# Kernel tuning notes

Measured on AMD Instinct MI355X. Metric: run time of the kernel, lower is better.

Reference implementation:

```python
import jax, jax.numpy as jnp
import numpy as np

B_, C, N, M, DX = 4, 8, 1024, 1024, 1
POINTS_PER_UNIT = 64


def setup_inputs() -> dict:
    key = jax.random.key(0)
    k1, k2, k3 = jax.random.split(key, 3)
    xz = jax.random.uniform(k1, (M, DX), dtype=jnp.float32)          # grid locations
    z = jax.random.normal(k2, (B_, C, M, M), dtype=jnp.float32)      # grid encoding
    x = jax.random.normal(k3, (B_, N, DX), dtype=jnp.float32)        # target locations
    log_scale = jnp.log(jnp.float32(2.0 / POINTS_PER_UNIT))          # learned scalar
    return {"xz": xz, "z": z, "x": x, "log_scale": log_scale}


def reference(xz, z, x, log_scale):
    # pairwise squared distances: (b, n, m)
    dists2 = jnp.sum((x[:, :, None, :] - xz[None, None, :, :]) ** 2, axis=-1)
    # RBF weights
    weights = jnp.exp(-0.5 * dists2 / jnp.exp(2.0 * log_scale))      # (b, n, m)
    # weighted interpolation of grid encoding: (b, c, n, m)
    z1 = jnp.einsum("bnm,bcmk->bcnk", weights, z)
    # outer product z1 @ z1^T: (b, c, n, n)
    z2 = jnp.einsum("bcnk,bcok->bcno", z1, z1)
    return (xz, z2)
```

## Files before the change

### kernel.cpp

```cpp
#include <hip/hip_runtime.h>
#include <hip/hip_bf16.h>


typedef __attribute__((ext_vector_type(8))) unsigned short u16x8;
typedef __attribute__((ext_vector_type(8))) __bf16 bf16x8;
typedef __attribute__((ext_vector_type(4))) float f32x4;

typedef __attribute__((address_space(1))) void gvoid;
typedef __attribute__((address_space(3))) void svoid;
#define GLDS(g, s) __builtin_amdgcn_global_load_lds((gvoid*)(g), (svoid*)(s), 16, 0, 0)
#define BAR() asm volatile("s_barrier" ::: "memory")

__device__ __forceinline__ unsigned short f2bf(float f) {
  unsigned int u = __builtin_bit_cast(unsigned int, f);
  u += 0x7fffu + ((u >> 16) & 1u);
  return (unsigned short)(u >> 16);
}

__device__ __forceinline__ bf16x8 as_bf16x8(u16x8 v) {
  return __builtin_bit_cast(bf16x8, v);
}

__global__ void weights_kernel(const float* __restrict__ xz, const float* __restrict__ x,
                               const float* __restrict__ ls, unsigned short* __restrict__ W) {
  int bn = blockIdx.x;
  float xv = x[bn];
  float coef = -0.5f * __expf(-2.0f * ls[0]);
  unsigned short* Wrow = W + (size_t)bn * 1024;
  #pragma unroll
  for (int i = 0; i < 4; ++i) {
    int m = threadIdx.x + i * 256;
    float d = xv - xz[m];
    Wrow[m] = f2bf(__expf(coef * d * d));
  }
}

__global__ void transpose_kernel(const float* __restrict__ Z, unsigned short* __restrict__ Zt) {
  __shared__ float tile[64][65];
  int bc = blockIdx.z;
  const float* Zp = Z + ((size_t)bc << 20);
  unsigned short* Ztp = Zt + ((size_t)bc << 20);
  int m0 = blockIdx.x * 64, k0 = blockIdx.y * 64;
  int tx = threadIdx.x & 63, tg = threadIdx.x >> 6;
  #pragma unroll
  for (int i = 0; i < 16; ++i) {
    int ml = tg + i * 4;
    tile[ml][tx] = Zp[(size_t)(m0 + ml) * 1024 + k0 + tx];
  }
  __syncthreads();
  int tx2 = (threadIdx.x & 31) * 2, kg = threadIdx.x >> 5;
  #pragma unroll
  for (int i = 0; i < 8; ++i) {
    int kl = kg + i * 8;
    ushort2 v;
    v.x = f2bf(tile[tx2][kl]);
    v.y = f2bf(tile[tx2 + 1][kl]);
    *(ushort2*)&Ztp[(size_t)(k0 + kl) * 1024 + m0 + tx2] = v;
  }
}

template<bool A_PER_B>
__global__ __launch_bounds__(512, 2)
void gemm_nt8(const unsigned short* __restrict__ A, const unsigned short* __restrict__ B,
              unsigned short* __restrict__ Cbf) {
  extern __shared__ __align__(16) char smem[];

  const int bid = blockIdx.x;
  const int w = ((bid & 7) << 6) + (bid >> 3);
  const int bc = w >> 4;
  const int t  = w & 15;
  const int bi = t & 3, bj = t >> 2;

  const unsigned short* Ap = A + ((size_t)(A_PER_B ? (bc >> 3) : bc) << 20);
  const unsigned short* Bp = B + ((size_t)bc << 20);
  const int tid = threadIdx.x;
  const int wv = tid >> 6, lane = tid & 63;
  const int wr = wv >> 2, wc = wv & 3;
  const int la = lane & 15, ha = lane >> 4;

  f32x4 acc[8][4] = {};

  const int slog = (lane & 7) ^ (lane >> 3);
  const int rloc = 2 * (lane >> 3) + (slog & 1);
  const int cloc = (slog >> 1) * 8;
  const unsigned short* gA0 = Ap + (size_t)(bi*256 +       wv*16 + rloc) * 1024 + cloc;
  const unsigned short* gA1 = Ap + (size_t)(bi*256 + 128 + wv*16 + rloc) * 1024 + cloc;
  const unsigned short* gB0 = Bp + (size_t)(bj*256 +       wv*16 + rloc) * 1024 + cloc;
  const unsigned short* gB1 = Bp + (size_t)(bj*256 + 128 + wv*16 + rloc) * 1024 + cloc;
  const int ldsw = wv * 1024;

  auto stageA = [&](int d, int kh, int kt) {
    const int ko = kt * 64 + kh * 32;
    char* dst = smem + d * 32768 + kh * 16384 + ldsw;
    GLDS(gA0 + ko, dst); GLDS(gA1 + ko, dst + 8192);
  };
  auto stageB = [&](int d, int kh, int kt) {
    const int ko = kt * 64 + kh * 32;
    char* dst = smem + 65536 + d * 32768 + kh * 16384 + ldsw;
    GLDS(gB0 + ko, dst); GLDS(gB1 + ko, dst + 8192);
  };

  const int sphys = ((ha << 1) | (la & 1)) ^ (la >> 1);
  const int abase = wr * 8192 + (la >> 1) * 128 + sphys * 16;
  const int bbase = 65536 + wc * 4096 + (la >> 1) * 128 + sphys * 16;

  u16x8 aX[4], aY[4], b0[4], b1[4];
  auto lda4 = [&](u16x8* dst, int d, int kh, int ms) {
    const char* p = smem + d * 32768 + kh * 16384 + ms * 4096 + abase;
    dst[0] = *(const u16x8*)(p);
    dst[1] = *(const u16x8*)(p + 1024);
    dst[2] = *(const u16x8*)(p + 2048);
    dst[3] = *(const u16x8*)(p + 3072);
  };
  auto ldb4 = [&](u16x8* dst, int d, int kh) {
    const char* p = smem + d * 32768 + kh * 16384 + bbase;
    dst[0] = *(const u16x8*)(p);
    dst[1] = *(const u16x8*)(p + 1024);
    dst[2] = *(const u16x8*)(p + 2048);
    dst[3] = *(const u16x8*)(p + 3072);
  };
  auto mfma16 = [&](const u16x8* Af, const u16x8* Bf, int ms) {
    __builtin_amdgcn_s_setprio(1);
    #pragma unroll
    for (int i = 0; i < 4; ++i)
      #pragma unroll
      for (int n = 0; n < 4; ++n)
        acc[ms * 4 + i][n] = __builtin_amdgcn_mfma_f32_16x16x32_bf16(
            as_bf16x8(Af[i]), as_bf16x8(Bf[n]), acc[ms * 4 + i][n], 0, 0, 0);
    __builtin_amdgcn_s_setprio(0);
  };

  stageA(0, 0, 0); stageB(0, 0, 0);
  stageA(0, 1, 0); stageB(0, 1, 0);
  stageA(1, 0, 1); stageB(1, 0, 1);
  asm volatile("s_waitcnt vmcnt(8)" ::: "memory");
  BAR();
  ldb4(b0, 0, 0); lda4(aX, 0, 0, 0);

  for (int tt = 0; tt < 14; ++tt) {
    const int d = tt & 1;
    stageA(d ^ 1, 1, tt + 1);
    lda4(aY, d, 0, 1);
    mfma16(aX, b0, 0);
    stageB(d ^ 1, 1, tt + 1);
    asm volatile("s_waitcnt vmcnt(8)" ::: "memory");
    BAR();
    ldb4(b1, d, 1); lda4(aX, d, 1, 0);
    mfma16(aY, b0, 1);
    stageA(d, 0, tt + 2);
    lda4(aY, d, 1, 1);
    mfma16(aX, b1, 0);
    stageB(d, 0, tt + 2);
    asm volatile("s_waitcnt vmcnt(8)" ::: "memory");
    BAR();
    ldb4(b0, d ^ 1, 0); lda4(aX, d ^ 1, 0, 0);
    mfma16(aY, b1, 1);
  }
  stageA(1, 1, 15);
  lda4(aY, 0, 0, 1);
  mfma16(aX, b0, 0);
  stageB(1, 1, 15);
  asm volatile("s_waitcnt vmcnt(8)" ::: "memory");
  BAR();
  ldb4(b1, 0, 1); lda4(aX, 0, 1, 0);
  mfma16(aY, b0, 1);
  lda4(aY, 0, 1, 1);
  mfma16(aX, b1, 0);
  asm volatile("s_waitcnt vmcnt(4)" ::: "memory");
  BAR();
  ldb4(b0, 1, 0); lda4(aX, 1, 0, 0);
  mfma16(aY, b1, 1);
  lda4(aY, 1, 0, 1);
  mfma16(aX, b0, 0);
  asm volatile("s_waitcnt vmcnt(0)" ::: "memory");
  BAR();
  ldb4(b1, 1, 1); lda4(aX, 1, 1, 0);
  mfma16(aY, b0, 1);
  lda4(aY, 1, 1, 1);
  mfma16(aX, b1, 0);
  mfma16(aY, b1, 1);
  BAR();

  const size_t cb20 = (size_t)bc << 20;
  unsigned short* sE = (unsigned short*)(smem) + wv * 1152;
  const int r2 = lane >> 2, ch = lane & 3;
  #pragma unroll
  for (int mb = 0; mb < 8; ++mb) {
    #pragma unroll
    for (int nb = 0; nb < 4; ++nb)
      #pragma unroll
      for (int j = 0; j < 4; ++j)
        sE[(ha * 4 + j) * 72 + nb * 16 + la] = f2bf(acc[mb][nb][j]);
    u16x8 v0 = *(const u16x8*)&sE[r2 * 72 + ch * 16];
    u16x8 v1 = *(const u16x8*)&sE[r2 * 72 + ch * 16 + 8];
    unsigned short* gp = Cbf + cb20 +
        (size_t)(bi * 256 + wr * 128 + mb * 16 + r2) * 1024 + bj * 256 + wc * 64 + ch * 16;
    *(u16x8*)gp = v0;
    *(u16x8*)(gp + 8) = v1;
  }
}

__global__ __launch_bounds__(256, 2)
void gemm2_sym(const unsigned short* __restrict__ A, float* __restrict__ Cf) {
  extern __shared__ __align__(16) char smem[];

  const int chunk = 80;
  int w = ((int)blockIdx.x & 7) * chunk + ((int)blockIdx.x >> 3);
  const int bc = w / 20;
  int t = w % 20;
  int bi, bj;
  if (t < 2)       { bj = 0; bi = t; }
  else if (t < 6)  { bj = 1; bi = t - 2; }
  else if (t < 12) { bj = 2; bi = t - 6; }
  else             { bj = 3; bi = t - 12; }

  const unsigned short* Ap = A + ((size_t)bc << 20);
  const int tid = threadIdx.x;
  const int wv = tid >> 6, lane = tid & 63;
  const int la = lane & 15, ha = lane >> 4;
  f32x4 acc[8][4] = {};

  const int slog = (lane & 7) ^ (lane >> 3);
  const int rloc = 2 * (lane >> 3) + (slog & 1);
  const int cloc = (slog >> 1) * 8;
  const unsigned short* gA0 = Ap + (size_t)(bi*128 + (wv     )*16 + rloc)*1024 + cloc;
  const unsigned short* gA1 = Ap + (size_t)(bi*128 + (wv +  4)*16 + rloc)*1024 + cloc;
  const unsigned short* gBq0 = Ap + (size_t)(bj*256 + (wv     )*16 + rloc)*1024 + cloc;
  const unsigned short* gBq1 = Ap + (size_t)(bj*256 + (wv +  4)*16 + rloc)*1024 + cloc;
  const unsigned short* gBq2 = Ap + (size_t)(bj*256 + (wv +  8)*16 + rloc)*1024 + cloc;
  const unsigned short* gBq3 = Ap + (size_t)(bj*256 + (wv + 12)*16 + rloc)*1024 + cloc;
  const int ldsw = wv * 1024;

  auto stage = [&](int slot, int kt) {
    char* base = smem + slot * 24576;
    GLDS(gA0 + kt, base + ldsw);
    GLDS(gA1 + kt, base + 4096 + ldsw);
    GLDS(gBq0 + kt, base + 8192  + ldsw);
    GLDS(gBq1 + kt, base + 12288 + ldsw);
    GLDS(gBq2 + kt, base + 16384 + ldsw);
    GLDS(gBq3 + kt, base + 20480 + ldsw);
  };

  const int sphys = ((ha << 1) | (la & 1)) ^ (la >> 1);
  const int roff = (la >> 1) * 128 + sphys * 16;

  u16x8 aX[8], bX[4], aY[8], bY[4];
  auto rd = [&](u16x8* da, u16x8* db, int slot) {
    const char* pa = smem + slot * 24576 + roff;
    #pragma unroll
    for (int mb = 0; mb < 8; ++mb) da[mb] = *(const u16x8*)(pa + mb * 1024);
    const char* pb = pa + 8192 + wv * 4096;
    #pragma unroll
    for (int nb = 0; nb < 4; ++nb) db[nb] = *(const u16x8*)(pb + nb * 1024);
  };
  auto mfma32 = [&](const u16x8* Af, const u16x8* Bf) {
    __builtin_amdgcn_s_setprio(1);
    #pragma unroll
    for (int mb = 0; mb < 8; ++mb)
      #pragma unroll
      for (int nb = 0; nb < 4; ++nb)
        acc[mb][nb] = __builtin_amdgcn_mfma_f32_16x16x32_bf16(
            as_bf16x8(Af[mb]), as_bf16x8(Bf[nb]), acc[mb][nb], 0, 0, 0);
    __builtin_amdgcn_s_setprio(0);
  };

  stage(0, 0); stage(1, 32); stage(2, 64);
  asm volatile("s_waitcnt vmcnt(6)" ::: "memory");
  BAR();
  rd(aX, bX, 0);
  asm volatile("s_waitcnt lgkmcnt(0)" ::: "memory");
  BAR();

  int p0 = 0, p1 = 1, p2 = 2;
  for (int t2 = 0; t2 < 28; t2 += 2) {
    stage(p0, (t2 + 3) * 32);
    rd(aY, bY, p1);
    mfma32(aX, bX);
    asm volatile("s_waitcnt vmcnt(6)" ::: "memory");
    BAR();
    stage(p1, (t2 + 4) * 32);
    rd(aX, bX, p2);
    mfma32(aY, bY);
    asm volatile("s_waitcnt vmcnt(6)" ::: "memory");
    BAR();
    int tmp = p2; p2 = p1; p1 = p0; p0 = tmp;
  }
  stage(p0, 31 * 32);
  rd(aY, bY, p1);
  mfma32(aX, bX);
  asm volatile("s_waitcnt vmcnt(6)" ::: "memory");
  BAR();
  rd(aX, bX, p2);
  mfma32(aY, bY);
  asm volatile("s_waitcnt vmcnt(0)" ::: "memory");
  BAR();
  rd(aY, bY, p0);
  mfma32(aX, bX);
  mfma32(aY, bY);
  BAR();

  const size_t cb20 = (size_t)bc << 20;

  {
    float* sF = (float*)(smem + wv * 5120);
    const int rr = lane >> 2, cch = (lane & 3) * 16;
    #pragma unroll
    for (int mb = 0; mb < 8; ++mb) {
      #pragma unroll
      for (int nb = 0; nb < 4; ++nb)
        #pragma unroll
        for (int j = 0; j < 4; ++j)
          sF[(ha * 4 + j) * 68 + nb * 16 + la] = acc[mb][nb][j];
      float* gp = Cf + cb20 +
          (size_t)(bi * 128 + mb * 16 + rr) * 1024 + bj * 256 + wv * 64 + cch;
      #pragma unroll
      for (int q = 0; q < 4; ++q)
        *(f32x4*)(gp + q * 4) = *(const f32x4*)&sF[rr * 68 + cch + q * 4];
    }
  }
  BAR();

  float (*sT)[129] = (float(*)[129])smem;
  #pragma unroll
  for (int h = 0; h < 2; ++h) {
    if (2 * bj + h >= 2 * (bi >> 1) + 2) {
      #pragma unroll
      for (int b = 0; b < 4; ++b) {
        if (wv == 2 * h + (b >> 1)) {
          const int nb0 = (b & 1) * 2;
          #pragma unroll
          for (int nn = 0; nn < 2; ++nn)
            #pragma unroll
            for (int mb = 0; mb < 8; ++mb)
              #pragma unroll
              for (int j = 0; j < 4; ++j)
                sT[nn * 16 + la][mb * 16 + ha * 4 + j] = acc[mb][nb0 + nn][j];
        }
        __syncthreads();
        const int sr = tid >> 3, cc = (tid & 7) * 16;
        float* gp = Cf + cb20 +
            (size_t)((2 * bj + h) * 128 + b * 32 + sr) * 1024 + bi * 128 + cc;
        #pragma unroll
        for (int q = 0; q < 4; ++q)
          *(f32x4*)(gp + q * 4) = *(const f32x4*)&sT[sr][cc + q * 4];
        __syncthreads();
      }
    }
  }
}

extern "C" void kernel_launch(void* const* d_in, const int* in_sizes, int n_in,
                              void* d_out, int out_size, void* d_ws, size_t ws_size,
                              hipStream_t stream) {
  const float* xz = (const float*)d_in[0];
  const float* z  = (const float*)d_in[1];
  const float* x  = (const float*)d_in[2];
  const float* ls = (const float*)d_in[3];
  float* out = (float*)d_out;

  unsigned short* W  = (unsigned short*)d_ws;
  unsigned short* Zt = W + ((size_t)4 << 20);
  unsigned short* z1 = Zt + ((size_t)32 << 20);

  hipFuncSetAttribute((const void*)gemm_nt8<true>,
                      hipFuncAttributeMaxDynamicSharedMemorySize, 131072);
  hipFuncSetAttribute((const void*)gemm2_sym,
                      hipFuncAttributeMaxDynamicSharedMemorySize, 73728);

  hipMemcpyAsync(out, xz, 1024 * sizeof(float), hipMemcpyDeviceToDevice, stream);
  weights_kernel<<<4096, 256, 0, stream>>>(xz, x, ls, W);
  transpose_kernel<<<dim3(16, 16, 32), 256, 0, stream>>>(z, Zt);
  gemm_nt8<true><<<512, 512, 131072, stream>>>(W, Zt, z1);
  gemm2_sym<<<640, 256, 73728, stream>>>(z1, out + 1024);
}
```

Before: 199.5 us.

## Split A-fragment LDS reads into half-tiles to cut register pressure in GEMM loop

Restructures the software pipeline of the z2 GEMM kernel so A fragments are read from LDS in two halves of four 16-row blocks, interleaved with 16-MFMA groups. This replaces the full double-buffered register fragments (aX/aY of 8) with smaller aP/aQ buffers, and shortens the global prefetch depth from three stages to two in flight. The aim is lower VGPR use and finer overlap of LDS reads with MFMA. The cost is more LDS read waves and a shallower global-load prefetch that may expose memory latency.

```diff
diff --git a/kernel.cpp b/kernel.cpp
--- a/kernel.cpp
+++ b/kernel.cpp
@@ -244,59 +244,65 @@
   const int sphys = ((ha << 1) | (la & 1)) ^ (la >> 1);
   const int roff = (la >> 1) * 128 + sphys * 16;
 
-  u16x8 aX[8], bX[4], aY[8], bY[4];
-  auto rd = [&](u16x8* da, u16x8* db, int slot) {
-    const char* pa = smem + slot * 24576 + roff;
-    #pragma unroll
-    for (int mb = 0; mb < 8; ++mb) da[mb] = *(const u16x8*)(pa + mb * 1024);
-    const char* pb = pa + 8192 + wv * 4096;
-    #pragma unroll
-    for (int nb = 0; nb < 4; ++nb) db[nb] = *(const u16x8*)(pb + nb * 1024);
-  };
-  auto mfma32 = [&](const u16x8* Af, const u16x8* Bf) {
+  u16x8 aP[4], aQ[4], bX[4], bY[4];
+  auto rdA = [&](u16x8* d, int slot, int ms) {
+    const char* pa = smem + slot * 24576 + ms * 4096 + roff;
+    d[0] = *(const u16x8*)(pa);
+    d[1] = *(const u16x8*)(pa + 1024);
+    d[2] = *(const u16x8*)(pa + 2048);
+    d[3] = *(const u16x8*)(pa + 3072);
+  };
+  auto rdB = [&](u16x8* d, int slot) {
+    const char* pb = smem + slot * 24576 + 8192 + wv * 4096 + roff;
+    d[0] = *(const u16x8*)(pb);
+    d[1] = *(const u16x8*)(pb + 1024);
+    d[2] = *(const u16x8*)(pb + 2048);
+    d[3] = *(const u16x8*)(pb + 3072);
+  };
+  auto mfma16 = [&](const u16x8* Af, const u16x8* Bf, int ms) {
     __builtin_amdgcn_s_setprio(1);
     #pragma unroll
-    for (int mb = 0; mb < 8; ++mb)
-      #pragma unroll
-      for (int nb = 0; nb < 4; ++nb)
-        acc[mb][nb] = __builtin_amdgcn_mfma_f32_16x16x32_bf16(
-            as_bf16x8(Af[mb]), as_bf16x8(Bf[nb]), acc[mb][nb], 0, 0, 0);
+    for (int i = 0; i < 4; ++i)
+      #pragma unroll
+      for (int n = 0; n < 4; ++n)
+        acc[ms * 4 + i][n] = __builtin_amdgcn_mfma_f32_16x16x32_bf16(
+            as_bf16x8(Af[i]), as_bf16x8(Bf[n]), acc[ms * 4 + i][n], 0, 0, 0);
     __builtin_amdgcn_s_setprio(0);
   };
 
-  stage(0, 0); stage(1, 32); stage(2, 64);
+  stage(0, 0); stage(1, 32);
   asm volatile("s_waitcnt vmcnt(6)" ::: "memory");
   BAR();
-  rd(aX, bX, 0);
-  asm volatile("s_waitcnt lgkmcnt(0)" ::: "memory");
-  BAR();
-
-  int p0 = 0, p1 = 1, p2 = 2;
-  for (int t2 = 0; t2 < 28; t2 += 2) {
-    stage(p0, (t2 + 3) * 32);
-    rd(aY, bY, p1);
-    mfma32(aX, bX);
+  rdB(bX, 0); rdA(aP, 0, 0);
+
+  int c0 = 0, c1 = 1, c2 = 2;
+  for (int it = 0; it < 15; ++it) {
+    const int t2 = it * 2;
+    rdA(aQ, c0, 1);
+    stage(c2, (t2 + 2) * 32);
+    mfma16(aP, bX, 0);
     asm volatile("s_waitcnt vmcnt(6)" ::: "memory");
     BAR();
-    stage(p1, (t2 + 4) * 32);
-    rd(aX, bX, p2);
-    mfma32(aY, bY);
+    rdB(bY, c1); rdA(aP, c1, 0);
+    mfma16(aQ, bX, 1);
+    rdA(aQ, c1, 1);
+    stage(c0, (t2 + 3) * 32);
+    mfma16(aP, bY, 0);
     asm volatile("s_waitcnt vmcnt(6)" ::: "memory");
     BAR();
-    int tmp = p2; p2 = p1; p1 = p0; p0 = tmp;
-  }
-  stage(p0, 31 * 32);
-  rd(aY, bY, p1);
-  mfma32(aX, bX);
-  asm volatile("s_waitcnt vmcnt(6)" ::: "memory");
-  BAR();
-  rd(aX, bX, p2);
-  mfma32(aY, bY);
+    rdB(bX, c2); rdA(aP, c2, 0);
+    mfma16(aQ, bY, 1);
+    int tmp = c0; c0 = c2; c2 = c1; c1 = tmp;
+  }
+  rdA(aQ, c0, 1);
+  mfma16(aP, bX, 0);
   asm volatile("s_waitcnt vmcnt(0)" ::: "memory");
   BAR();
-  rd(aY, bY, p0);
-  mfma32(aX, bX);
-  mfma32(aY, bY);
+  rdB(bY, c1); rdA(aP, c1, 0);
+  mfma16(aQ, bX, 1);
+  rdA(aQ, c1, 1);
+  mfma16(aP, bY, 0);
+  mfma16(aQ, bY, 1);
   BAR();
 
   const size_t cb20 = (size_t)bc << 20;
```

Result: faster. 191.4 us (-4.1%).
